# Performance work log

Hardware: AMD Instinct MI355X
Metric: run time of the kernel (lower is better)

## Reference

```python
import jax, jax.numpy as jnp
import numpy as np

S = 64        # FARGAN_SUBFRAME_SIZE
NSUB = 4      # FARGAN_SUBFRAMES
HOP = 256     # HOPSIZE = NSUB * S
NF = 256      # num_features
GC = 256      # global_channels
IC = NF + GC  # input_channels
B = 64
T = 100

NOISE_KEY = jax.random.key(1)


def _w(k, shape):
    return jax.random.normal(k, shape, dtype=jnp.float32) / np.sqrt(shape[-1]).astype(np.float32)


def setup_inputs() -> dict:
    key = jax.random.key(0)
    ks = jax.random.split(key, 20)
    return {
        'features': jax.random.normal(ks[0], (B, NF, T), dtype=jnp.float32),
        'global_features': jax.random.normal(ks[1], (B, GC, 1), dtype=jnp.float32),
        'in_W1': _w(ks[2], (IC, IC)),
        'in_b1': jnp.zeros((IC,), jnp.float32),
        'in_W2': _w(ks[3], (HOP, IC)),
        'in_b2': jnp.zeros((HOP,), jnp.float32),
        'fw_W': _w(ks[4], (S, 2 * S)),
        'fw_glu_W': _w(ks[5], (S, S)),
        'gru1_Wih': _w(ks[6], (3 * S, 2 * S)),
        'gru1_Whh': _w(ks[7], (3 * S, S)),
        'glu1_W': _w(ks[8], (S, S)),
        'gru2_Wih': _w(ks[9], (3 * S, 2 * S)),
        'gru2_Whh': _w(ks[10], (3 * S, S)),
        'glu2_W': _w(ks[11], (S, S)),
        'gru3_Wih': _w(ks[12], (3 * S, 2 * S)),
        'gru3_Whh': _w(ks[13], (3 * S, S)),
        'glu3_W': _w(ks[14], (S, S)),
        'skip_dense_W': _w(ks[15], (2 * S, 5 * S)),
        'skip_glu_W': _w(ks[16], (2 * S, 2 * S)),
        'out_W': _w(ks[17], (S, 2 * S)),
    }


def _noise(x, k):
    return jnp.clip(x + (jax.random.uniform(k, x.shape, x.dtype) - 0.5) * (1.0 / 127.0), -1.0, 1.0)


def _glu(x, W):
    return x * jax.nn.sigmoid(x @ W.T)


def _gru_cell(x, h, Wih, Whh):
    gi = x @ Wih.T  # [B, 3S]
    gh = h @ Whh.T
    i_r, i_z, i_n = jnp.split(gi, 3, axis=-1)
    h_r, h_z, h_n = jnp.split(gh, 3, axis=-1)
    r = jax.nn.sigmoid(i_r + h_r)
    z = jax.nn.sigmoid(i_z + h_z)
    n = jnp.tanh(i_n + r * h_n)
    return (1.0 - z) * n + z * h


def _forward(features, global_features, in_W1, in_b1, in_W2, in_b2, fw_W, fw_glu_W,
             gru1_Wih, gru1_Whh, glu1_W, gru2_Wih, gru2_Whh, glu2_W,
             gru3_Wih, gru3_Whh, glu3_W, skip_dense_W, skip_glu_W, out_W):
    b = features.shape[0]
    t = features.shape[2]
    g = global_features[:, :, 0]  # [B, GC]

    def subframe_step(sub, prev, st, key):
        h1, h2, h3, s3 = st
        kk = jax.random.split(key, 10)
        sub = _noise(sub, kk[0])
        prev = _noise(prev, kk[1])
        fw = _noise(_glu(jnp.tanh(jnp.concatenate([sub, s3], -1) @ fw_W.T), fw_glu_W), kk[2])
        h1n = _gru_cell(jnp.concatenate([fw, prev], -1), h1, gru1_Wih, gru1_Whh)
        g1 = _noise(_glu(_noise(h1n, kk[3]), glu1_W), kk[4])
        h2n = _gru_cell(jnp.concatenate([g1, prev], -1), h2, gru2_Wih, gru2_Whh)
        g2 = _noise(_glu(_noise(h2n, kk[5]), glu2_W), kk[6])
        h3n = _gru_cell(jnp.concatenate([g2, prev], -1), h3, gru3_Wih, gru3_Whh)
        g3 = _noise(_glu(_noise(h3n, kk[7]), glu3_W), kk[8])
        skip_feats = jnp.concatenate([g1, g2, g3, fw, prev], -1)  # [B, 5S]
        skip = _glu(_noise(jnp.tanh(skip_feats @ skip_dense_W.T), kk[9]), skip_glu_W)
        out = jnp.tanh(skip @ out_W.T)  # [B, S]
        return out, (h1n, h2n, h3n, sub)

    def frame_step(carry, f_t):
        st, prev, i = carry
        x = jnp.tanh(jnp.concatenate([f_t, g], -1) @ in_W1.T + in_b1) @ in_W2.T + in_b2  # [B, HOP]
        outs = []
        for s in range(NSUB):
            k = jax.random.fold_in(NOISE_KEY, i * NSUB + s)
            o, st = subframe_step(x[:, s * S:(s + 1) * S], prev, st, k)
            prev = o
            outs.append(o)
        return (st, prev, i + 1), jnp.concatenate(outs, -1)

    z = jnp.zeros((b, S), features.dtype)
    init = ((z, z, z, z), z, jnp.int32(0))
    xs = jnp.transpose(features, (2, 0, 1))  # [T, B, NF]
    _, ys = jax.lax.scan(frame_step, init, xs)  # [T, B, HOP]
    signal = jnp.transpose(ys, (1, 0, 2)).reshape(b, t * HOP)
    return signal[:, None, :]  # [B, 1, T*HOP]


def reference(features, global_features, in_W1, in_b1, in_W2, in_b2, fw_W, fw_glu_W,
              gru1_Wih, gru1_Whh, glu1_W, gru2_Wih, gru2_Whh, glu2_W,
              gru3_Wih, gru3_Whh, glu3_W, skip_dense_W, skip_glu_W, out_W):
    return _forward(features, global_features, in_W1, in_b1, in_W2, in_b2, fw_W, fw_glu_W,
                    gru1_Wih, gru1_Whh, glu1_W, gru2_Wih, gru2_Whh, glu2_W,
                    gru3_Wih, gru3_Whh, glu3_W, skip_dense_W, skip_glu_W, out_W)
```

## Files before the change

### kernel.cpp

```cpp
#include <hip/hip_runtime.h>
#include <stdint.h>

#define SS 64
#define BB 64
#define TT 100
#define HOPC 256
#define NFC 256
#define GCC 256
#define ICC 512
#define NC (1.0f/127.0f)
#define NBLK 64
#define NTHR 512

#define OFF_FW     0
#define OFF_FWGLU  8192
#define OFF_G1IH   12288
#define OFF_G1HH   36864
#define OFF_GLU1   49152
#define OFF_G2IH   53248
#define OFF_G2HH   77824
#define OFF_GLU2   90112
#define OFF_G3IH   94208
#define OFF_G3HH   118784
#define OFF_GLU3   131072
#define OFF_SKIPD  135168
#define OFF_SKIPG  176128
#define OFF_OUT    192512
#define W_TOTAL    200704
#define XALL_F32   (TT * BB * HOPC)
#define UG_FLOATS  ((size_t)400 * 64 * 704)

typedef _Float16 f16;
typedef _Float16 h2 __attribute__((ext_vector_type(2)));
union U16 { uint4 u; h2 h[4]; };

#if __has_builtin(__builtin_amdgcn_fdot2)
#define FDOT2(a, b, c) __builtin_amdgcn_fdot2((a), (b), (c), false)
#else
#define FDOT2(a, b, c) ((c) + (float)(a)[0] * (float)(b)[0] + (float)(a)[1] * (float)(b)[1])
#endif

__device__ __forceinline__ uint32_t rotl32(uint32_t x, int r) {
    return (x << r) | (x >> (32 - r));
}

__device__ __forceinline__ void tf2x32(uint32_t k0, uint32_t k1, uint32_t c0, uint32_t c1,
                                       uint32_t& o0, uint32_t& o1) {
    uint32_t k2 = k0 ^ k1 ^ 0x1BD11BDAu;
    uint32_t x0 = c0 + k0, x1 = c1 + k1;
    x0 += x1; x1 = rotl32(x1, 13); x1 ^= x0;
    x0 += x1; x1 = rotl32(x1, 15); x1 ^= x0;
    x0 += x1; x1 = rotl32(x1, 26); x1 ^= x0;
    x0 += x1; x1 = rotl32(x1, 6);  x1 ^= x0;
    x0 += k1; x1 += k2 + 1u;
    x0 += x1; x1 = rotl32(x1, 17); x1 ^= x0;
    x0 += x1; x1 = rotl32(x1, 29); x1 ^= x0;
    x0 += x1; x1 = rotl32(x1, 16); x1 ^= x0;
    x0 += x1; x1 = rotl32(x1, 24); x1 ^= x0;
    x0 += k2; x1 += k0 + 2u;
    x0 += x1; x1 = rotl32(x1, 13); x1 ^= x0;
    x0 += x1; x1 = rotl32(x1, 15); x1 ^= x0;
    x0 += x1; x1 = rotl32(x1, 26); x1 ^= x0;
    x0 += x1; x1 = rotl32(x1, 6);  x1 ^= x0;
    x0 += k0; x1 += k1 + 3u;
    x0 += x1; x1 = rotl32(x1, 17); x1 ^= x0;
    x0 += x1; x1 = rotl32(x1, 29); x1 ^= x0;
    x0 += x1; x1 = rotl32(x1, 16); x1 ^= x0;
    x0 += x1; x1 = rotl32(x1, 24); x1 ^= x0;
    x0 += k1; x1 += k2 + 4u;
    x0 += x1; x1 = rotl32(x1, 13); x1 ^= x0;
    x0 += x1; x1 = rotl32(x1, 15); x1 ^= x0;
    x0 += x1; x1 = rotl32(x1, 26); x1 ^= x0;
    x0 += x1; x1 = rotl32(x1, 6);  x1 ^= x0;
    x0 += k2; x1 += k0 + 5u;
    o0 = x0; o1 = x1;
}

__device__ __forceinline__ float unifP(uint32_t k0, uint32_t k1, uint32_t m) {
    uint32_t o0, o1;
    tf2x32(k0, k1, 0u, m, o0, o1);
    uint32_t bits = o0 ^ o1;
    return __uint_as_float((bits >> 9) | 0x3f800000u) - 1.0f;
}

__device__ __forceinline__ float clipf(float v) { return fminf(1.0f, fmaxf(-1.0f, v)); }
__device__ __forceinline__ float noiseu(float v, float u) {
    return clipf(v + (u - 0.5f) * NC);
}
__device__ __forceinline__ float sigmf(float v) {
    return __fdividef(1.0f, 1.0f + __expf(-v));
}
__device__ __forceinline__ float tanhfast(float x) {
    float ax = fminf(fabsf(x), 15.0f);
    float e = __expf(2.0f * ax);
    float r = __fdividef(e - 1.0f, e + 1.0f);
    return copysignf(r, x);
}

__device__ __forceinline__ void bar_lds() {
    asm volatile("s_waitcnt lgkmcnt(0)\n\ts_barrier" ::: "memory");
}

__device__ __forceinline__ float red8dpp(float v) {
    int t;
    t = __builtin_amdgcn_update_dpp(0, __float_as_int(v), 0xB1, 0xF, 0xF, true);
    v += __int_as_float(t);
    t = __builtin_amdgcn_update_dpp(0, __float_as_int(v), 0x4E, 0xF, 0xF, true);
    v += __int_as_float(t);
    t = __builtin_amdgcn_update_dpp(0, __float_as_int(v), 0x141, 0xF, 0xF, true);
    v += __int_as_float(t);
    return v;
}

__device__ __forceinline__ float dotU(const U16& w, const U16& x, float acc) {
#pragma unroll
    for (int i = 0; i < 4; ++i) acc = FDOT2(w.h[i], x.h[i], acc);
    return acc;
}

struct WF1  { U16 w[2]; };
struct WGRU { U16 wih[6]; U16 whh[3]; U16 glu; };
struct WSK  { U16 w[10]; };
struct WSG  { U16 w[4]; };

__device__ __forceinline__ void ldF1(const f16* W, int row, int g, WF1& r) {
    const f16* p = W + row * 128 + g * 16;
    r.w[0].u = *(const uint4*)p;
    r.w[1].u = *(const uint4*)(p + 8);
}
__device__ __forceinline__ void ldF2(const f16* W, int row, int g, U16& r) {
    r.u = *(const uint4*)(W + row * 64 + g * 8);
}
__device__ __forceinline__ void ldGRU(const f16* Wih, const f16* Whh, const f16* Glu,
                                      int row, int g, WGRU& r) {
#pragma unroll
    for (int j = 0; j < 3; ++j) {
        const f16* p = Wih + (row + 64 * j) * 128 + g * 16;
        r.wih[2 * j].u     = *(const uint4*)p;
        r.wih[2 * j + 1].u = *(const uint4*)(p + 8);
        r.whh[j].u = *(const uint4*)(Whh + (row + 64 * j) * 64 + g * 8);
    }
    r.glu.u = *(const uint4*)(Glu + row * 64 + g * 8);
}
__device__ __forceinline__ void ldSK(const f16* W, int row, int g, WSK& r) {
#pragma unroll
    for (int j = 0; j < 2; ++j) {
        const f16* p = W + (row + 64 * j) * 320 + g * 40;
#pragma unroll
        for (int i = 0; i < 5; ++i) r.w[5 * j + i].u = *(const uint4*)(p + 8 * i);
    }
}
__device__ __forceinline__ void ldSG(const f16* W, int row, int g, WSG& r) {
#pragma unroll
    for (int j = 0; j < 2; ++j) {
        const f16* p = W + (row + 64 * j) * 128 + g * 16;
        r.w[2 * j].u     = *(const uint4*)p;
        r.w[2 * j + 1].u = *(const uint4*)(p + 8);
    }
}

__device__ __forceinline__ void pinU(U16& r) {
    asm volatile("" : "+v"(r.u.x), "+v"(r.u.y), "+v"(r.u.z), "+v"(r.u.w));
}

struct SrcW { const float* p[14]; };

__global__ __launch_bounds__(256) void fargan_cvtw(SrcW s, f16* __restrict__ dst) {
    const int offs[15] = {0, 8192, 12288, 36864, 49152, 53248, 77824, 90112,
                          94208, 118784, 131072, 135168, 176128, 192512, 200704};
    int i = blockIdx.x * 256 + threadIdx.x;
    if (i >= W_TOTAL) return;
    int sgi = 0;
#pragma unroll
    for (int t = 1; t < 14; ++t) sgi += (i >= offs[t]);
    dst[i] = (f16)s.p[sgi][i - offs[sgi]];
}

__global__ __launch_bounds__(256) void fargan_tr(const float* __restrict__ f,
                                                 float* __restrict__ fT) {
    __shared__ float L[64][104];
    int b = blockIdx.x >> 2, c0 = (blockIdx.x & 3) * 64;
    for (int e = threadIdx.x; e < 6400; e += 256) {
        int r = e / 100, col = e - r * 100;
        L[r][col] = f[b * NFC * TT + (c0 + r) * TT + col];
    }
    __syncthreads();
    for (int e = threadIdx.x; e < 6400; e += 256) {
        int t = e >> 6, c = e & 63;
        fT[(t * BB + b) * NFC + c0 + c] = L[c][t];
    }
}

__global__ __launch_bounds__(256) void fargan_frame(
    const float* __restrict__ fT, const float* __restrict__ gfeat,
    const float* __restrict__ W1, const float* __restrict__ ib1,
    const float* __restrict__ W2, const float* __restrict__ ib2,
    float* __restrict__ xall)
{
    __shared__ __align__(16) float cat[16][ICC];
    __shared__ __align__(16) float zb[16][ICC];
    const int tid = threadIdx.x;
    const int t = blockIdx.x >> 2;
    const int q = blockIdx.x & 3;

    for (int bb = 0; bb < 16; ++bb) {
        int b = q * 16 + bb;
        for (int c = tid; c < ICC; c += 256) {
            float v = (c < NFC) ? fT[(t * BB + b) * NFC + c]
                                : gfeat[b * GCC + (c - NFC)];
            cat[bb][c] = v;
        }
    }
    __syncthreads();

    {
        int rg = tid & 63, bg = tid >> 6;
        int n0 = rg * 8, bb0 = bg * 4;
        float acc[8][4];
#pragma unroll
        for (int r = 0; r < 8; ++r)
#pragma unroll
            for (int j = 0; j < 4; ++j) acc[r][j] = 0.f;
        for (int k = 0; k < ICC; k += 4) {
            float4 cv[4];
#pragma unroll
            for (int j = 0; j < 4; ++j) cv[j] = *(const float4*)&cat[bb0 + j][k];
#pragma unroll
            for (int r = 0; r < 8; ++r) {
                float4 wv = *(const float4*)&W1[(n0 + r) * ICC + k];
#pragma unroll
                for (int j = 0; j < 4; ++j)
                    acc[r][j] += wv.x * cv[j].x + wv.y * cv[j].y + wv.z * cv[j].z + wv.w * cv[j].w;
            }
        }
#pragma unroll
        for (int r = 0; r < 8; ++r) {
            float bias = ib1[n0 + r];
#pragma unroll
            for (int j = 0; j < 4; ++j)
                zb[bb0 + j][n0 + r] = tanhf(acc[r][j] + bias);
        }
    }
    __syncthreads();

    {
        int rg = tid & 63, bg = tid >> 6;
        int n0 = rg * 4, bb0 = bg * 4;
        float acc[4][4];
#pragma unroll
        for (int r = 0; r < 4; ++r)
#pragma unroll
            for (int j = 0; j < 4; ++j) acc[r][j] = 0.f;
        for (int k = 0; k < ICC; k += 4) {
            float4 cv[4];
#pragma unroll
            for (int j = 0; j < 4; ++j) cv[j] = *(const float4*)&zb[bb0 + j][k];
#pragma unroll
            for (int r = 0; r < 4; ++r) {
                float4 wv = *(const float4*)&W2[(n0 + r) * ICC + k];
#pragma unroll
                for (int j = 0; j < 4; ++j)
                    acc[r][j] += wv.x * cv[j].x + wv.y * cv[j].y + wv.z * cv[j].z + wv.w * cv[j].w;
            }
        }
#pragma unroll
        for (int r = 0; r < 4; ++r) {
            float bias = ib2[n0 + r];
#pragma unroll
            for (int j = 0; j < 4; ++j) {
                int b = q * 16 + bb0 + j;
                xall[(t * BB + b) * HOPC + n0 + r] = acc[r][j] + bias;
            }
        }
    }
}

__global__ __launch_bounds__(256) void fargan_ugen(float* __restrict__ ug) {
    __shared__ uint32_t kk[20];
    const int idx = blockIdx.x;
    const int tid = threadIdx.x;
    if (tid < 10) {
        uint32_t f0, f1; tf2x32(0u, 1u, 0u, (uint32_t)idx, f0, f1);
        uint32_t A, Bv;  tf2x32(f0, f1, 0u, (uint32_t)tid, A, Bv);
        kk[2 * tid] = A; kk[2 * tid + 1] = Bv;
    }
    __syncthreads();
    float* dst = ug + (size_t)idx * 64 * 704;
    for (int c = 0; c < 64; ++c) {
        for (int j = tid; j < 704; j += 256) {
            int sl = j >> 6;
            int kx = (sl < 9) ? 2 * sl : 18;
            uint32_t m = (sl < 9) ? (uint32_t)(c * 64 + (j & 63))
                                  : (uint32_t)(c * 128 + (j - 576));
            dst[c * 704 + j] = unifP(kk[kx], kk[kx + 1], m);
        }
    }
}

__global__ __launch_bounds__(512) void fargan_seqpg(
    const float* __restrict__ xall, const f16* __restrict__ wh,
    const float* __restrict__ ug, float* __restrict__ outp)
{
    const int tid = threadIdx.x;
    const int row = tid >> 3;
    const int g = tid & 7;
    const int bg = blockIdx.x;

    __shared__ __align__(16) f16 XH[128];
    __shared__ __align__(16) f16 SKXH[320];
    __shared__ __align__(16) f16 TWH[64], HNH[64];
    __shared__ __align__(16) f16 SPNH[128], SKVH[128];
    __shared__ __align__(16) f16 HH[2][3][64];
    __shared__ __align__(16) float Hf[2][3][64];
    __shared__ __align__(16) float UNF[2][704];

    WF1 rF1;  ldF1(wh + OFF_FW, row, g, rF1);
    U16 rF2;  ldF2(wh + OFF_FWGLU, row, g, rF2);
    WGRU rG1; ldGRU(wh + OFF_G1IH, wh + OFF_G1HH, wh + OFF_GLU1, row, g, rG1);
    WGRU rG2; ldGRU(wh + OFF_G2IH, wh + OFF_G2HH, wh + OFF_GLU2, row, g, rG2);
    WGRU rG3; ldGRU(wh + OFF_G3IH, wh + OFF_G3HH, wh + OFF_GLU3, row, g, rG3);
    WSG rSG;  ldSG(wh + OFF_SKIPG, row, g, rSG);
    WF1 rOUT; ldF1(wh + OFF_OUT, row, g, rOUT);

    pinU(rF1.w[0]); pinU(rF1.w[1]); pinU(rF2);
#pragma unroll
    for (int j = 0; j < 6; ++j) { pinU(rG1.wih[j]); pinU(rG2.wih[j]); pinU(rG3.wih[j]); }
#pragma unroll
    for (int j = 0; j < 3; ++j) { pinU(rG1.whh[j]); pinU(rG2.whh[j]); pinU(rG3.whh[j]); }
    pinU(rG1.glu); pinU(rG2.glu); pinU(rG3.glu);
#pragma unroll
    for (int j = 0; j < 4; ++j) pinU(rSG.w[j]);
    pinU(rOUT.w[0]); pinU(rOUT.w[1]);

    float prevO = 0.f, xs_old = 0.f;
    if (g == 0) {
#pragma unroll
        for (int i = 0; i < 3; ++i) { Hf[0][i][row] = 0.f; HH[0][i][row] = (f16)0.f; }
        XH[row] = (f16)0.f; XH[64 + row] = (f16)0.f;
    }

    for (int j = tid; j < 704; j += NTHR)
        UNF[0][j] = ug[(size_t)bg * 704 + j];

    float xf0 = xall[(0 * BB + bg) * HOPC + 0 * SS + row];
    float xf1 = xall[(0 * BB + bg) * HOPC + 1 * SS + row];
    float xf2 = xall[(0 * BB + bg) * HOPC + 2 * SS + row];
    float xf3 = xall[(0 * BB + bg) * HOPC + 3 * SS + row];
    __syncthreads();

    for (int t = 0; t < TT; ++t) {
        const int tn = (t + 1 < TT) ? t + 1 : t;
        float xn0 = xall[(tn * BB + bg) * HOPC + 0 * SS + row];
        float xn1 = xall[(tn * BB + bg) * HOPC + 1 * SS + row];
        float xn2 = xall[(tn * BB + bg) * HOPC + 2 * SS + row];
        float xn3 = xall[(tn * BB + bg) * HOPC + 3 * SS + row];

        for (int s = 0; s < 4; ++s) {
            const int idx = t * 4 + s;
            const int p = idx & 1;
            float gl0, gl1;

            if (g == 0) {
                float u0 = UNF[p][row];
                float u1 = UNF[p][64 + row];
                float xv = (s == 0) ? xf0 : (s == 1) ? xf1 : (s == 2) ? xf2 : xf3;
                float xs = noiseu(xv, u0);
                XH[row] = (f16)xs; XH[64 + row] = (f16)xs_old; xs_old = xs;
                SKXH[256 + row] = (f16)noiseu(prevO, u1);
            }
            bar_lds();

            float twv;
            {
                const int idn = (idx + 1 < 400) ? idx + 1 : 399;
                const float* gsrc = ug + ((size_t)idn * 64 + bg) * 704;
                gl0 = gsrc[tid];
                gl1 = (tid < 192) ? gsrc[512 + tid] : 0.f;

                U16 xa, xb;
                xa.u = *(const uint4*)&XH[g * 16];
                xb.u = *(const uint4*)&XH[g * 16 + 8];
                float a = dotU(rF1.w[0], xa, 0.f);
                a = dotU(rF1.w[1], xb, a);
                twv = tanhfast(red8dpp(a));
                if (g == 0) TWH[row] = (f16)twv;
            }
            bar_lds();

            {
                U16 xa; xa.u = *(const uint4*)&TWH[g * 8];
                float a = red8dpp(dotU(rF2, xa, 0.f));
                if (g == 0) SKXH[192 + row] = (f16)noiseu(twv * sigmf(a), UNF[p][128 + row]);
            }
            bar_lds();

#define GRU_STEP(RG, XPTR, GI, UH, UG_, GOFF, EXTRA)                                        \
            {                                                                               \
                const f16* xin = (XPTR);                                                    \
                U16 xa, xb, xh;                                                             \
                xa.u = *(const uint4*)xin;                                                  \
                xb.u = *(const uint4*)(xin + 8);                                            \
                xh.u = *(const uint4*)&HH[p][GI][g * 8];                                    \
                EXTRA;                                                                      \
                float ai0 = 0, ai1 = 0, ai2 = 0, ah0 = 0, ah1 = 0, ah2 = 0;                 \
                ai0 = dotU(RG.wih[0], xa, ai0); ai0 = dotU(RG.wih[1], xb, ai0);             \
                ai1 = dotU(RG.wih[2], xa, ai1); ai1 = dotU(RG.wih[3], xb, ai1);             \
                ai2 = dotU(RG.wih[4], xa, ai2); ai2 = dotU(RG.wih[5], xb, ai2);             \
                ah0 = dotU(RG.whh[0], xh, ah0);                                             \
                ah1 = dotU(RG.whh[1], xh, ah1);                                             \
                ah2 = dotU(RG.whh[2], xh, ah2);                                             \
                ai0 = red8dpp(ai0); ai1 = red8dpp(ai1); ai2 = red8dpp(ai2);                 \
                ah0 = red8dpp(ah0); ah1 = red8dpp(ah1); ah2 = red8dpp(ah2);                 \
                float hold = Hf[p][GI][row];                                                \
                float r  = sigmf(ai0 + ah0);                                                \
                float z  = sigmf(ai1 + ah1);                                                \
                float nn = tanhfast(ai2 + r * ah2);                                         \
                float hnew = (1.f - z) * nn + z * hold;                                     \
                float hNv = noiseu(hnew, UNF[p][(UH) + row]);                               \
                if (g == 0) {                                                               \
                    Hf[p ^ 1][GI][row] = hnew;                                              \
                    HH[p ^ 1][GI][row] = (f16)hnew;                                         \
                    HNH[row] = (f16)hNv;                                                    \
                }                                                                           \
                bar_lds();                                                                  \
                U16 xg; xg.u = *(const uint4*)&HNH[g * 8];                                  \
                float ag = red8dpp(dotU(RG.glu, xg, 0.f));                                  \
                if (g == 0) SKXH[(GOFF) + row] =                                            \
                    (f16)noiseu(hNv * sigmf(ag), UNF[p][(UG_) + row]);                      \
            }                                                                               \
            bar_lds();

#define UNF_STORE do {                                                                      \
                UNF[p ^ 1][tid] = gl0;                                                      \
                if (tid < 192) UNF[p ^ 1][512 + tid] = gl1; } while (0)

            GRU_STEP(rG1, SKXH + 192 + g * 16, 0, 192, 256, 0, ((void)0))
            GRU_STEP(rG2, (g < 4 ? SKXH + g * 16 : SKXH + 256 + (g - 4) * 16), 1, 320, 384, 64, UNF_STORE)
            WSK rSK; ldSK(wh + OFF_SKIPD, row, g, rSK);
            GRU_STEP(rG3, (g < 4 ? SKXH + 64 + g * 16 : SKXH + 256 + (g - 4) * 16), 2, 448, 512, 128, ((void)0))
#undef GRU_STEP
#undef UNF_STORE

            float sp0, sp1;
            {
                U16 xs[5];
#pragma unroll
                for (int i = 0; i < 5; ++i) xs[i].u = *(const uint4*)&SKXH[g * 40 + 8 * i];
                float a0 = 0, a1 = 0;
#pragma unroll
                for (int i = 0; i < 5; ++i) {
                    a0 = dotU(rSK.w[i], xs[i], a0);
                    a1 = dotU(rSK.w[5 + i], xs[i], a1);
                }
                sp0 = noiseu(tanhfast(red8dpp(a0)), UNF[p][576 + row]);
                sp1 = noiseu(tanhfast(red8dpp(a1)), UNF[p][640 + row]);
                if (g == 0) { SPNH[row] = (f16)sp0; SPNH[64 + row] = (f16)sp1; }
            }
            bar_lds();

            {
                U16 xa, xb;
                xa.u = *(const uint4*)&SPNH[g * 16];
                xb.u = *(const uint4*)&SPNH[g * 16 + 8];
                float a0 = dotU(rSG.w[0], xa, 0.f); a0 = dotU(rSG.w[1], xb, a0);
                float a1 = dotU(rSG.w[2], xa, 0.f); a1 = dotU(rSG.w[3], xb, a1);
                a0 = red8dpp(a0); a1 = red8dpp(a1);
                if (g == 0) {
                    SKVH[row]      = (f16)(sp0 * sigmf(a0));
                    SKVH[64 + row] = (f16)(sp1 * sigmf(a1));
                }
            }
            bar_lds();

            {
                U16 xa, xb;
                xa.u = *(const uint4*)&SKVH[g * 16];
                xb.u = *(const uint4*)&SKVH[g * 16 + 8];
                float a = dotU(rOUT.w[0], xa, 0.f);
                a = dotU(rOUT.w[1], xb, a);
                float o = tanhfast(red8dpp(a));
                prevO = o;
                if (g == 0) outp[bg * (TT * HOPC) + t * HOPC + s * SS + row] = o;
            }
        }
        xf0 = xn0; xf1 = xn1; xf2 = xn2; xf3 = xn3;
    }
}

__global__ __launch_bounds__(512) void fargan_seq(
    const float* __restrict__ xall, const f16* __restrict__ wh,
    float* __restrict__ outp)
{
    const int tid = threadIdx.x;
    const int row = tid >> 3;
    const int g = tid & 7;
    const int bg = blockIdx.x;

    __shared__ __align__(16) f16 XH[128];
    __shared__ __align__(16) f16 SKXH[320];
    __shared__ __align__(16) f16 TWH[64], HNH[64];
    __shared__ __align__(16) f16 SPNH[128], SKVH[128];
    __shared__ __align__(16) f16 HH[2][3][64];
    __shared__ __align__(16) float Hf[2][3][64];
    __shared__ __align__(16) float UNF[2][704];
    __shared__ uint32_t KK[401][20];

    WF1 rF1;  ldF1(wh + OFF_FW, row, g, rF1);
    U16 rF2;  ldF2(wh + OFF_FWGLU, row, g, rF2);
    WGRU rG1; ldGRU(wh + OFF_G1IH, wh + OFF_G1HH, wh + OFF_GLU1, row, g, rG1);
    WGRU rG2; ldGRU(wh + OFF_G2IH, wh + OFF_G2HH, wh + OFF_GLU2, row, g, rG2);
    WGRU rG3; ldGRU(wh + OFF_G3IH, wh + OFF_G3HH, wh + OFF_GLU3, row, g, rG3);
    WSG rSG;  ldSG(wh + OFF_SKIPG, row, g, rSG);
    WF1 rOUT; ldF1(wh + OFF_OUT, row, g, rOUT);

    pinU(rF1.w[0]); pinU(rF1.w[1]); pinU(rF2);
#pragma unroll
    for (int j = 0; j < 6; ++j) { pinU(rG1.wih[j]); pinU(rG2.wih[j]); pinU(rG3.wih[j]); }
#pragma unroll
    for (int j = 0; j < 3; ++j) { pinU(rG1.whh[j]); pinU(rG2.whh[j]); pinU(rG3.whh[j]); }
    pinU(rG1.glu); pinU(rG2.glu); pinU(rG3.glu);
#pragma unroll
    for (int j = 0; j < 4; ++j) pinU(rSG.w[j]);
    pinU(rOUT.w[0]); pinU(rOUT.w[1]);

    float prevO = 0.f, xs_old = 0.f;
    if (g == 0) {
#pragma unroll
        for (int i = 0; i < 3; ++i) { Hf[0][i][row] = 0.f; HH[0][i][row] = (f16)0.f; }
        XH[row] = (f16)0.f; XH[64 + row] = (f16)0.f;
    }

    for (int e = tid; e < 4010; e += NTHR) {
        int ii = e / 10, ki = e - ii * 10;
        uint32_t f0, f1; tf2x32(0u, 1u, 0u, (uint32_t)ii, f0, f1);
        uint32_t A, Bv;  tf2x32(f0, f1, 0u, (uint32_t)ki, A, Bv);
        KK[ii][2 * ki] = A; KK[ii][2 * ki + 1] = Bv;
    }
    __syncthreads();

    for (int j = tid; j < 704; j += NTHR) {
        int sl = j >> 6;
        int kx = (sl < 9) ? 2 * sl : 18;
        uint32_t m = (sl < 9) ? (uint32_t)(bg * 64 + (j & 63))
                              : (uint32_t)(bg * 128 + (j - 576));
        UNF[0][j] = unifP(KK[0][kx], KK[0][kx + 1], m);
    }

    float xf0 = xall[(0 * BB + bg) * HOPC + 0 * SS + row];
    float xf1 = xall[(0 * BB + bg) * HOPC + 1 * SS + row];
    float xf2 = xall[(0 * BB + bg) * HOPC + 2 * SS + row];
    float xf3 = xall[(0 * BB + bg) * HOPC + 3 * SS + row];
    __syncthreads();

    for (int t = 0; t < TT; ++t) {
        const int tn = (t + 1 < TT) ? t + 1 : t;
        float xn0 = xall[(tn * BB + bg) * HOPC + 0 * SS + row];
        float xn1 = xall[(tn * BB + bg) * HOPC + 1 * SS + row];
        float xn2 = xall[(tn * BB + bg) * HOPC + 2 * SS + row];
        float xn3 = xall[(tn * BB + bg) * HOPC + 3 * SS + row];

        for (int s = 0; s < 4; ++s) {
            const int idx = t * 4 + s;
            const int p = idx & 1;

            if (g == 0) {
                float u0 = UNF[p][row];
                float u1 = UNF[p][64 + row];
                float xv = (s == 0) ? xf0 : (s == 1) ? xf1 : (s == 2) ? xf2 : xf3;
                float xs = noiseu(xv, u0);
                XH[row] = (f16)xs; XH[64 + row] = (f16)xs_old; xs_old = xs;
                SKXH[256 + row] = (f16)noiseu(prevO, u1);
            }
            bar_lds();

            float twv;
            {
                U16 xa, xb;
                xa.u = *(const uint4*)&XH[g * 16];
                xb.u = *(const uint4*)&XH[g * 16 + 8];
                float a = dotU(rF1.w[0], xa, 0.f);
                a = dotU(rF1.w[1], xb, a);
                twv = tanhfast(red8dpp(a));
                if (g == 0) TWH[row] = (f16)twv;
            }
            bar_lds();

            {
                U16 xa; xa.u = *(const uint4*)&TWH[g * 8];
                if (tid < 256) {
                    int kx = 2 * (tid >> 6);
                    UNF[p ^ 1][tid] = unifP(KK[idx + 1][kx], KK[idx + 1][kx + 1],
                                            (uint32_t)(bg * 64 + (tid & 63)));
                }
                float a = red8dpp(dotU(rF2, xa, 0.f));
                if (g == 0) SKXH[192 + row] = (f16)noiseu(twv * sigmf(a), UNF[p][128 + row]);
            }
            bar_lds();

#define GRU_STEP(RG, XPTR, GI, UH, UG_, GOFF, EXTRA)                                        \
            {                                                                               \
                const f16* xin = (XPTR);                                                    \
                U16 xa, xb, xh;                                                             \
                xa.u = *(const uint4*)xin;                                                  \
                xb.u = *(const uint4*)(xin + 8);                                            \
                xh.u = *(const uint4*)&HH[p][GI][g * 8];                                    \
                EXTRA;                                                                      \
                float ai0 = 0, ai1 = 0, ai2 = 0, ah0 = 0, ah1 = 0, ah2 = 0;                 \
                ai0 = dotU(RG.wih[0], xa, ai0); ai0 = dotU(RG.wih[1], xb, ai0);             \
                ai1 = dotU(RG.wih[2], xa, ai1); ai1 = dotU(RG.wih[3], xb, ai1);             \
                ai2 = dotU(RG.wih[4], xa, ai2); ai2 = dotU(RG.wih[5], xb, ai2);             \
                ah0 = dotU(RG.whh[0], xh, ah0);                                             \
                ah1 = dotU(RG.whh[1], xh, ah1);                                             \
                ah2 = dotU(RG.whh[2], xh, ah2);                                             \
                ai0 = red8dpp(ai0); ai1 = red8dpp(ai1); ai2 = red8dpp(ai2);                 \
                ah0 = red8dpp(ah0); ah1 = red8dpp(ah1); ah2 = red8dpp(ah2);                 \
                float hold = Hf[p][GI][row];                                                \
                float r  = sigmf(ai0 + ah0);                                                \
                float z  = sigmf(ai1 + ah1);                                                \
                float nn = tanhfast(ai2 + r * ah2);                                         \
                float hnew = (1.f - z) * nn + z * hold;                                     \
                float hNv = noiseu(hnew, UNF[p][(UH) + row]);                               \
                if (g == 0) {                                                               \
                    Hf[p ^ 1][GI][row] = hnew;                                              \
                    HH[p ^ 1][GI][row] = (f16)hnew;                                         \
                    HNH[row] = (f16)hNv;                                                    \
                }                                                                           \
                bar_lds();                                                                  \
                U16 xg; xg.u = *(const uint4*)&HNH[g * 8];                                  \
                float ag = red8dpp(dotU(RG.glu, xg, 0.f));                                  \
                if (g == 0) SKXH[(GOFF) + row] =                                            \
                    (f16)noiseu(hNv * sigmf(ag), UNF[p][(UG_) + row]);                      \
            }                                                                               \
            bar_lds();

#define NOISE_A2 do { if (tid >= 256) {                                                     \
                int kx = 2 * (tid >> 6);                                                    \
                UNF[p ^ 1][tid] = unifP(KK[idx + 1][kx], KK[idx + 1][kx + 1],               \
                                        (uint32_t)(bg * 64 + (tid & 63))); } } while (0)
#define NOISE_B do { int j2 = tid + 512; if (j2 < 704) {                                    \
                int kx = (j2 < 576) ? 16 : 18;                                              \
                uint32_t m2 = (j2 < 576) ? (uint32_t)(bg * 64 + (j2 & 63))                  \
                                         : (uint32_t)(bg * 128 + (j2 - 576));               \
                UNF[p ^ 1][j2] = unifP(KK[idx + 1][kx], KK[idx + 1][kx + 1], m2); } } while (0)

            GRU_STEP(rG1, SKXH + 192 + g * 16, 0, 192, 256, 0, NOISE_A2)
            GRU_STEP(rG2, (g < 4 ? SKXH + g * 16 : SKXH + 256 + (g - 4) * 16), 1, 320, 384, 64, NOISE_B)
            WSK rSK; ldSK(wh + OFF_SKIPD, row, g, rSK);
            GRU_STEP(rG3, (g < 4 ? SKXH + 64 + g * 16 : SKXH + 256 + (g - 4) * 16), 2, 448, 512, 128, ((void)0))
#undef GRU_STEP
#undef NOISE_A2
#undef NOISE_B

            float sp0, sp1;
            {
                U16 xs[5];
#pragma unroll
                for (int i = 0; i < 5; ++i) xs[i].u = *(const uint4*)&SKXH[g * 40 + 8 * i];
                float a0 = 0, a1 = 0;
#pragma unroll
                for (int i = 0; i < 5; ++i) {
                    a0 = dotU(rSK.w[i], xs[i], a0);
                    a1 = dotU(rSK.w[5 + i], xs[i], a1);
                }
                sp0 = noiseu(tanhfast(red8dpp(a0)), UNF[p][576 + row]);
                sp1 = noiseu(tanhfast(red8dpp(a1)), UNF[p][640 + row]);
                if (g == 0) { SPNH[row] = (f16)sp0; SPNH[64 + row] = (f16)sp1; }
            }
            bar_lds();

            {
                U16 xa, xb;
                xa.u = *(const uint4*)&SPNH[g * 16];
                xb.u = *(const uint4*)&SPNH[g * 16 + 8];
                float a0 = dotU(rSG.w[0], xa, 0.f); a0 = dotU(rSG.w[1], xb, a0);
                float a1 = dotU(rSG.w[2], xa, 0.f); a1 = dotU(rSG.w[3], xb, a1);
                a0 = red8dpp(a0); a1 = red8dpp(a1);
                if (g == 0) {
                    SKVH[row]      = (f16)(sp0 * sigmf(a0));
                    SKVH[64 + row] = (f16)(sp1 * sigmf(a1));
                }
            }
            bar_lds();

            {
                U16 xa, xb;
                xa.u = *(const uint4*)&SKVH[g * 16];
                xb.u = *(const uint4*)&SKVH[g * 16 + 8];
                float a = dotU(rOUT.w[0], xa, 0.f);
                a = dotU(rOUT.w[1], xb, a);
                float o = tanhfast(red8dpp(a));
                prevO = o;
                if (g == 0) outp[bg * (TT * HOPC) + t * HOPC + s * SS + row] = o;
            }
        }
        xf0 = xn0; xf1 = xn1; xf2 = xn2; xf3 = xn3;
    }
}

extern "C" void kernel_launch(void* const* d_in, const int* in_sizes, int n_in,
                              void* d_out, int out_size, void* d_ws, size_t ws_size,
                              hipStream_t stream) {
    const float* features = (const float*)d_in[0];
    const float* gfeat    = (const float*)d_in[1];
    const float* W1       = (const float*)d_in[2];
    const float* ib1      = (const float*)d_in[3];
    const float* W2       = (const float*)d_in[4];
    const float* ib2      = (const float*)d_in[5];

    float* xall = (float*)d_ws;
    float* fT   = xall + XALL_F32;
    f16*   wh   = (f16*)(fT + XALL_F32);
    float* ug   = (float*)(wh + W_TOTAL);
    float* outp = (float*)d_out;

    const size_t need = (size_t)13508608 + UG_FLOATS * 4;
    const bool pregen = (ws_size >= need);

    SrcW sw;
    for (int i = 0; i < 14; ++i) sw.p[i] = (const float*)d_in[6 + i];

    hipLaunchKernelGGL(fargan_cvtw, dim3((W_TOTAL + 255) / 256), dim3(256), 0, stream, sw, wh);
    hipLaunchKernelGGL(fargan_tr, dim3(256), dim3(256), 0, stream, features, fT);
    hipLaunchKernelGGL(fargan_frame, dim3(TT * 4), dim3(256), 0, stream,
                       fT, gfeat, W1, ib1, W2, ib2, xall);
    if (pregen) {
        hipLaunchKernelGGL(fargan_ugen, dim3(400), dim3(256), 0, stream, ug);
        hipLaunchKernelGGL(fargan_seqpg, dim3(NBLK), dim3(NTHR), 0, stream,
                           xall, wh, ug, outp);
    } else {
        hipLaunchKernelGGL(fargan_seq, dim3(NBLK), dim3(NTHR), 0, stream, xall, wh, outp);
    }
}
```

Measured before the change: 2.562 ms.

## Retile frame MLP kernel with LDS-staged weight tiles and more blocks

```diff
diff --git a/kernel.cpp b/kernel.cpp
--- a/kernel.cpp
+++ b/kernel.cpp
@@ -197,81 +197,69 @@
     const float* __restrict__ W2, const float* __restrict__ ib2,
     float* __restrict__ xall)
 {
-    __shared__ __align__(16) float cat[16][ICC];
-    __shared__ __align__(16) float zb[16][ICC];
+    __shared__ __align__(16) float catL[8 * 516];
+    __shared__ __align__(16) float zbL[8 * 516];
+    __shared__ __align__(16) float Wt[64 * 68];
     const int tid = threadIdx.x;
-    const int t = blockIdx.x >> 2;
-    const int q = blockIdx.x & 3;
-
-    for (int bb = 0; bb < 16; ++bb) {
-        int b = q * 16 + bb;
-        for (int c = tid; c < ICC; c += 256) {
-            float v = (c < NFC) ? fT[(t * BB + b) * NFC + c]
-                                : gfeat[b * GCC + (c - NFC)];
-            cat[bb][c] = v;
+    const int t = blockIdx.x >> 3;
+    const int q = blockIdx.x & 7;
+    const int b = tid & 7;
+    const int nq = tid >> 3;
+
+    for (int e = tid; e < 8 * 512; e += 256) {
+        int bb = e >> 9, c = e & 511;
+        float v = (c < NFC) ? fT[(t * BB + q * 8 + bb) * NFC + c]
+                            : gfeat[(q * 8 + bb) * GCC + (c - NFC)];
+        catL[bb * 516 + c] = v;
+    }
+    __syncthreads();
+
+    for (int n0 = 0; n0 < 512; n0 += 64) {
+        float a0 = 0.f, a1 = 0.f;
+        for (int k0 = 0; k0 < 512; k0 += 64) {
+            for (int e = tid; e < 1024; e += 256) {
+                int r = e >> 4, c4 = (e & 15) << 2;
+                *(float4*)&Wt[r * 68 + c4] =
+                    *(const float4*)&W1[(n0 + r) * ICC + k0 + c4];
+            }
+            __syncthreads();
+#pragma unroll
+            for (int kc = 0; kc < 16; ++kc) {
+                float4 cv = *(const float4*)&catL[b * 516 + k0 + kc * 4];
+                float4 w0 = *(const float4*)&Wt[nq * 68 + kc * 4];
+                float4 w1 = *(const float4*)&Wt[(nq + 32) * 68 + kc * 4];
+                a0 += w0.x * cv.x + w0.y * cv.y + w0.z * cv.z + w0.w * cv.w;
+                a1 += w1.x * cv.x + w1.y * cv.y + w1.z * cv.z + w1.w * cv.w;
+            }
+            __syncthreads();
         }
+        zbL[b * 516 + n0 + nq]      = tanhf(a0 + ib1[n0 + nq]);
+        zbL[b * 516 + n0 + nq + 32] = tanhf(a1 + ib1[n0 + nq + 32]);
     }
     __syncthreads();
 
-    {
-        int rg = tid & 63, bg = tid >> 6;
-        int n0 = rg * 8, bb0 = bg * 4;
-        float acc[8][4];
-#pragma unroll
-        for (int r = 0; r < 8; ++r)
-#pragma unroll
-            for (int j = 0; j < 4; ++j) acc[r][j] = 0.f;
-        for (int k = 0; k < ICC; k += 4) {
-            float4 cv[4];
-#pragma unroll
-            for (int j = 0; j < 4; ++j) cv[j] = *(const float4*)&cat[bb0 + j][k];
-#pragma unroll
-            for (int r = 0; r < 8; ++r) {
-                float4 wv = *(const float4*)&W1[(n0 + r) * ICC + k];
-#pragma unroll
-                for (int j = 0; j < 4; ++j)
-                    acc[r][j] += wv.x * cv[j].x + wv.y * cv[j].y + wv.z * cv[j].z + wv.w * cv[j].w;
-            }
+    for (int n0 = 0; n0 < 256; n0 += 64) {
+        float a0 = 0.f, a1 = 0.f;
+        for (int k0 = 0; k0 < 512; k0 += 64) {
+            for (int e = tid; e < 1024; e += 256) {
+                int r = e >> 4, c4 = (e & 15) << 2;
+                *(float4*)&Wt[r * 68 + c4] =
+                    *(const float4*)&W2[(n0 + r) * ICC + k0 + c4];
+            }
+            __syncthreads();
+#pragma unroll
+            for (int kc = 0; kc < 16; ++kc) {
+                float4 cv = *(const float4*)&zbL[b * 516 + k0 + kc * 4];
+                float4 w0 = *(const float4*)&Wt[nq * 68 + kc * 4];
+                float4 w1 = *(const float4*)&Wt[(nq + 32) * 68 + kc * 4];
+                a0 += w0.x * cv.x + w0.y * cv.y + w0.z * cv.z + w0.w * cv.w;
+                a1 += w1.x * cv.x + w1.y * cv.y + w1.z * cv.z + w1.w * cv.w;
+            }
+            __syncthreads();
         }
-#pragma unroll
-        for (int r = 0; r < 8; ++r) {
-            float bias = ib1[n0 + r];
-#pragma unroll
-            for (int j = 0; j < 4; ++j)
-                zb[bb0 + j][n0 + r] = tanhf(acc[r][j] + bias);
-        }
-    }
-    __syncthreads();
-
-    {
-        int rg = tid & 63, bg = tid >> 6;
-        int n0 = rg * 4, bb0 = bg * 4;
-        float acc[4][4];
-#pragma unroll
-        for (int r = 0; r < 4; ++r)
-#pragma unroll
-            for (int j = 0; j < 4; ++j) acc[r][j] = 0.f;
-        for (int k = 0; k < ICC; k += 4) {
-            float4 cv[4];
-#pragma unroll
-            for (int j = 0; j < 4; ++j) cv[j] = *(const float4*)&zb[bb0 + j][k];
-#pragma unroll
-            for (int r = 0; r < 4; ++r) {
-                float4 wv = *(const float4*)&W2[(n0 + r) * ICC + k];
-#pragma unroll
-                for (int j = 0; j < 4; ++j)
-                    acc[r][j] += wv.x * cv[j].x + wv.y * cv[j].y + wv.z * cv[j].z + wv.w * cv[j].w;
-            }
-        }
-#pragma unroll
-        for (int r = 0; r < 4; ++r) {
-            float bias = ib2[n0 + r];
-#pragma unroll
-            for (int j = 0; j < 4; ++j) {
-                int b = q * 16 + bb0 + j;
-                xall[(t * BB + b) * HOPC + n0 + r] = acc[r][j] + bias;
-            }
-        }
+        int B = t * BB + q * 8 + b;
+        xall[B * HOPC + n0 + nq]      = a0 + ib2[n0 + nq];
+        xall[B * HOPC + n0 + nq + 32] = a1 + ib2[n0 + nq + 32];
     }
 }
 
@@ -617,7 +605,7 @@
                 float hold = Hf[p][GI][row];                                                \
                 float r  = sigmf(ai0 + ah0);                                                \
                 float z  = sigmf(ai1 + ah1);                                                \
-                float nn = tanhfast(ai2 + r * ah2);                                         \
+                float nn = tanhfast(ai2 + r * ah2);                                        \
                 float hnew = (1.f - z) * nn + z * hold;                                     \
                 float hNv = noiseu(hnew, UNF[p][(UH) + row]);                               \
                 if (g == 0) {                                                               \
@@ -721,7 +709,7 @@
 
     hipLaunchKernelGGL(fargan_cvtw, dim3((W_TOTAL + 255) / 256), dim3(256), 0, stream, sw, wh);
     hipLaunchKernelGGL(fargan_tr, dim3(256), dim3(256), 0, stream, features, fT);
-    hipLaunchKernelGGL(fargan_frame, dim3(TT * 4), dim3(256), 0, stream,
+    hipLaunchKernelGGL(fargan_frame, dim3(TT * 8), dim3(256), 0, stream,
                        fT, gfeat, W1, ib1, W2, ib2, xall);
     if (pregen) {
         hipLaunchKernelGGL(fargan_ugen, dim3(400), dim3(256), 0, stream, ug);
```

After: 2.363 ms. 7.8% less time.
